# Performance work log

Hardware: AMD Instinct MI355X
Metric: run time of the kernel (lower is better)

The kernel has to match this reference:

```python
import jax, jax.numpy as jnp
import numpy as np

N = 64        # n_nodes per graph
H = 128       # hidden channels (128x0e + 128x1o)
NB = 8        # radial bessel basis size
L = 2         # num_interactions
R_MAX = 5.0
AVG_NEIGH = 63.0
DIM = 3       # output vector dim
B = 64        # batch (vmapped)
T = 32        # time-embedding dim
S = 5         # num_species


def _edges(n):
    # fully-connected graph, no self loops (static shapes, jit-friendly)
    s, r = np.meshgrid(np.arange(n), np.arange(n), indexing='ij')
    m = s != r
    return jnp.asarray(s[m]), jnp.asarray(r[m])


def setup_inputs() -> dict:
    key = jax.random.key(0)
    ks = jax.random.split(key, 12)
    sc = 0.05
    return {
        'positions': jax.random.normal(ks[0], (B, N, 3), jnp.float32),
        'node_features': jax.random.randint(ks[1], (B, N), 0, S).astype(jnp.int64),
        'global_features': jax.random.normal(ks[2], (B, T), jnp.float32),
        'emb': jax.random.normal(ks[3], (S, H), jnp.float32) * sc,
        'Wt': jax.random.normal(ks[4], (T, H), jnp.float32) * sc,
        'Wr1': jax.random.normal(ks[5], (L, NB, H), jnp.float32) * sc,
        'Wr2': jax.random.normal(ks[6], (L, H, H), jnp.float32) * sc,
        'Wupd': jax.random.normal(ks[7], (L, H, H), jnp.float32) * sc,
        'Wmix': jax.random.normal(ks[8], (L, H, H), jnp.float32) * sc,
        'Wg1': jax.random.normal(ks[9], (H, H), jnp.float32) * sc,
        'Wg2': jax.random.normal(ks[10], (H, H), jnp.float32) * sc,
        'final_scaling': jnp.ones((), jnp.float32),
    }


def _call_single(pos, z, t, emb, Wt, Wr1, Wr2, Wupd, Wmix, Wg1, Wg2, final_scaling):
    snd, rcv = _edges(N)
    ev = pos[rcv] - pos[snd]                               # [E,3] edge vectors (gather)
    r = jnp.sqrt(jnp.sum(ev * ev, axis=-1) + 1e-12)        # [E]
    u = ev / r[:, None]                                    # unit directions
    # Bessel radial basis with cosine cutoff (r_max acts as soft radius graph)
    n = jnp.arange(1, NB + 1, dtype=pos.dtype)
    rb = jnp.sin(n * jnp.pi * r[:, None] / R_MAX) / r[:, None]   # [E,NB]
    fc = 0.5 * (jnp.cos(jnp.pi * r / R_MAX) + 1.0) * (r < R_MAX)
    rb = rb * fc[:, None]
    # node embedding from species + time embedding
    h = emb[z] + t @ Wt                                    # [N,H] scalar features
    v = jnp.zeros((N, H, DIM), pos.dtype)                  # vector (1o) features
    for l in range(L):
        w = jax.nn.silu(rb @ Wr1[l]) @ Wr2[l]              # [E,H] radial weights
        m0 = w * h[snd]                                    # [E,H] scalar messages
        m1 = m0[:, :, None] * u[:, None, :]                # [E,H,3] vector messages
        a0 = jax.ops.segment_sum(m0, rcv, num_segments=N) / AVG_NEIGH
        a1 = jax.ops.segment_sum(m1, rcv, num_segments=N) / AVG_NEIGH
        h = h + a0 @ Wupd[l]
        v = v + jnp.einsum('ngd,gh->nhd', a1, Wmix[l])
    # equivariant readout: scalar gate per channel contracts vector channels
    g = jax.nn.silu(h @ Wg1) @ Wg2                         # [N,H]
    out = jnp.einsum('nhd,nh->nd', v, g)                   # [N,3]
    return out * final_scaling


def reference(positions, node_features, global_features, emb, Wt, Wr1, Wr2, Wupd, Wmix, Wg1, Wg2, final_scaling):
    f = lambda p, z, t: _call_single(p, z, t, emb, Wt, Wr1, Wr2, Wupd, Wmix, Wg1, Wg2, final_scaling)
    return jax.vmap(f)(positions, node_features, global_features)
```

## Files before the change

kernel.cpp:

```cpp
#include <hip/hip_runtime.h>
#include <math.h>

#define NN 64
#define HH 128
#define NBB 8
#define TT 32
#define BB 64
#define NROW (BB * NN)
#define PLANE ((size_t)NROW * HH)
#define WR1OFF (8 * 16384)

typedef __attribute__((ext_vector_type(8))) short short8;
typedef __attribute__((ext_vector_type(4))) float f32x4;
typedef __attribute__((ext_vector_type(2))) float f32x2;

__device__ __forceinline__ float silu_f(float x) {
  return x * __builtin_amdgcn_rcpf(1.0f + __expf(-x));
}

__device__ __forceinline__ unsigned short bf1(float x) {
  __bf16 h = (__bf16)x;
  return *(unsigned short*)&h;
}
__device__ __forceinline__ unsigned bf2(float lo, float hi) {
  return (unsigned)bf1(lo) | ((unsigned)bf1(hi) << 16);
}

__device__ __forceinline__ void gemm8(
    const unsigned short (*sA)[136], const unsigned short* __restrict__ Bp,
    int w, int nlo, int quad, f32x4 C[2]) {
  const short8 z8 = {0, 0, 0, 0, 0, 0, 0, 0};
  short8 afr[4];
#pragma unroll
  for (int kt = 0; kt < 4; ++kt)
    afr[kt] = (nlo < 8) ? *(const short8*)&sA[nlo][kt * 32 + quad * 8] : z8;
#pragma unroll
  for (int nt = 0; nt < 2; ++nt)
#pragma unroll
    for (int kt = 0; kt < 4; ++kt) {
      short8 bfr = *(const short8*)&Bp[((kt * 128 + w * 32 + nt * 16 + nlo) * 4 + quad) * 8];
      C[nt] = __builtin_amdgcn_mfma_f32_16x16x32_bf16(afr[kt], bfr, C[nt], 0, 0, 0);
    }
}

__global__ __launch_bounds__(256) void k_init(
    const float* __restrict__ emb, const int* __restrict__ z,
    const float* __restrict__ gf, const float* __restrict__ Wt,
    const float* __restrict__ Wr1, const float* __restrict__ Wr2,
    const float* __restrict__ Wupd, const float* __restrict__ Wmix,
    const float* __restrict__ Wg1, const float* __restrict__ Wg2,
    float* __restrict__ h, unsigned short* __restrict__ Wpack) {
  __shared__ float tvec[HH];
  __shared__ int sz[NN];
  int b4 = blockIdx.x, tid = threadIdx.x;
#pragma unroll
  for (int ii = 0; ii < 2; ++ii) {
    int idx = b4 * 512 + ii * 256 + tid;
    int m = idx >> 14;
    int local = idx & 16383;
    float val;
    if (m < 2) val = Wr2[idx];
    else if (m < 4) val = Wupd[idx - 32768];
    else if (m < 6) val = Wmix[idx - 65536];
    else if (m == 6) val = Wg1[local];
    else val = Wg2[local];
    int k = local >> 7, n = local & 127;
    int kt = k >> 5, q = (k >> 3) & 3, j = k & 7;
    Wpack[(idx & ~16383) + (((kt * 128 + n) * 4 + q) * 8) + j] = bf1(val);
  }
  if (tid < 32) {
    int e = b4 * 32 + tid;
    int l = e >> 12, p = e & 4095;
    int n = p >> 5, q = (p >> 3) & 3, j = p & 7;
    float val = (q == 0) ? Wr1[l * NBB * HH + j * HH + n] : 0.f;
    Wpack[WR1OFF + l * 4096 + p] = bf1(val);
  }
  if (b4 < 64) {
    int b = b4;
    if (tid < NN) sz[tid] = z[b * NN + tid];
    if (tid < HH) {
      float acc = 0.f;
#pragma unroll
      for (int k = 0; k < TT; ++k) acc += gf[b * TT + k] * Wt[k * HH + tid];
      tvec[tid] = acc;
    }
    __syncthreads();
    for (int i = tid; i < NN * HH; i += 256) {
      int n = i >> 7, c = i & 127;
      h[(size_t)b * NN * HH + i] = emb[sz[n] * HH + c] + tvec[c];
    }
  }
}

__global__ __launch_bounds__(256) void k_layer(
    const float* __restrict__ pos,
    const float* __restrict__ hA,
    const unsigned short* __restrict__ a0in,
    unsigned short* __restrict__ apout,
    const unsigned short* __restrict__ Wpack,
    int l) {
  __shared__ __align__(16) unsigned short sh_S[NN][136];
  __shared__ __align__(16) unsigned short sh_rbh[2][NN][8];
  __shared__ __align__(16) float sh_u[2][3][NN];

  int blk = blockIdx.x;
  int b = blk >> 5, rp = blk & 31;
  int r0 = rp * 2;
  int tid = threadIdx.x;
  int w = tid >> 6, lane = tid & 63;
  int nlo = lane & 15, quad = lane >> 4;

  f32x4 hbv[4][2];
#pragma unroll
  for (int mt = 0; mt < 4; ++mt)
#pragma unroll
    for (int nt = 0; nt < 2; ++nt)
#pragma unroll
      for (int reg = 0; reg < 4; ++reg)
        hbv[mt][nt][reg] =
            hA[((size_t)b * NN + mt * 16 + quad * 4 + reg) * HH + w * 32 + nt * 16 + nlo];

  {
    int s = tid & 63;
    int ksel = (tid >> 6) & 1;
    int ri = (tid >> 7) & 1;
    int r = r0 + ri;
    const float* pb = pos + b * NN * 3;
    float dx = pb[r * 3 + 0] - pb[s * 3 + 0];
    float dy = pb[r * 3 + 1] - pb[s * 3 + 1];
    float dz = pb[r * 3 + 2] - pb[s * 3 + 2];
    float rr = sqrtf(dx * dx + dy * dy + dz * dz + 1e-12f);
    float inv = __builtin_amdgcn_rcpf(rr);
    if (ksel == 0) {
      sh_u[ri][0][s] = dx * inv; sh_u[ri][1][s] = dy * inv; sh_u[ri][2][s] = dz * inv;
    }
    const float PI_OVER_5 = 0.628318530717958647692f;
    float fc = (s != r && rr < 5.0f) ? 0.5f * (__cosf(PI_OVER_5 * rr) + 1.0f) : 0.0f;
    float base = PI_OVER_5 * rr;
    float sc = inv * fc;
    int k0 = ksel * 4;
    float v0 = __sinf((float)(k0 + 1) * base) * sc;
    float v1 = __sinf((float)(k0 + 2) * base) * sc;
    float v2 = __sinf((float)(k0 + 3) * base) * sc;
    float v3 = __sinf((float)(k0 + 4) * base) * sc;
    *(unsigned*)&sh_rbh[ri][s][k0]     = bf2(v0, v1);
    *(unsigned*)&sh_rbh[ri][s][k0 + 2] = bf2(v2, v3);
  }
  if (l) {
    for (int i = tid; i < NN * 64; i += 256) {
      int s = i >> 6, c2 = (i & 63) * 2;
      *(unsigned*)&sh_S[s][c2] =
          *(const unsigned*)&a0in[((size_t)b * NN + s) * HH + c2];
    }
  }
  __syncthreads();

  if (l) {
    const unsigned short* Bu = Wpack + 2 * 16384;
#pragma unroll
    for (int mt = 0; mt < 4; ++mt) {
      short8 afr[4];
#pragma unroll
      for (int kt = 0; kt < 4; ++kt)
        afr[kt] = *(const short8*)&sh_S[mt * 16 + nlo][kt * 32 + quad * 8];
#pragma unroll
      for (int nt = 0; nt < 2; ++nt)
#pragma unroll
        for (int kt = 0; kt < 4; ++kt) {
          short8 bfr = *(const short8*)&Bu[((kt * 128 + w * 32 + nt * 16 + nlo) * 4 + quad) * 8];
          hbv[mt][nt] = __builtin_amdgcn_mfma_f32_16x16x32_bf16(afr[kt], bfr, hbv[mt][nt], 0, 0, 0);
        }
    }
    __syncthreads();
  }

  const unsigned short* Wr1p = Wpack + WR1OFF + l * 4096;
  short8 bw[2];
#pragma unroll
  for (int nt = 0; nt < 2; ++nt)
    bw[nt] = *(const short8*)&Wr1p[((w * 32 + nt * 16 + nlo) * 4 + quad) * 8];
  const unsigned short* Bbase = Wpack + l * 16384;
  short8 bfr[4][2];
#pragma unroll
  for (int kt = 0; kt < 4; ++kt)
#pragma unroll
    for (int nt = 0; nt < 2; ++nt)
      bfr[kt][nt] = *(const short8*)&Bbase[((kt * 128 + w * 32 + nt * 16 + nlo) * 4 + quad) * 8];

  const short8 zero8 = {0, 0, 0, 0, 0, 0, 0, 0};
  const float invAvg = 1.0f / 63.0f;

#pragma unroll
  for (int ri = 0; ri < 2; ++ri) {
#pragma unroll
    for (int mtp = 0; mtp < 2; ++mtp) {
      f32x4 Cs[2][2];
#pragma unroll
      for (int mi = 0; mi < 2; ++mi)
#pragma unroll
        for (int nt = 0; nt < 2; ++nt) Cs[mi][nt] = (f32x4){0.f, 0.f, 0.f, 0.f};
#pragma unroll
      for (int mi = 0; mi < 2; ++mi) {
        int mt = mtp * 2 + mi;
        short8 afr = (quad == 0) ? *(const short8*)&sh_rbh[ri][mt * 16 + nlo][0] : zero8;
#pragma unroll
        for (int nt = 0; nt < 2; ++nt)
          Cs[mi][nt] = __builtin_amdgcn_mfma_f32_16x16x32_bf16(afr, bw[nt], Cs[mi][nt], 0, 0, 0);
      }
#pragma unroll
      for (int mi = 0; mi < 2; ++mi)
#pragma unroll
        for (int nt = 0; nt < 2; ++nt)
#pragma unroll
          for (int reg = 0; reg < 4; ++reg) {
            int s = (mtp * 2 + mi) * 16 + quad * 4 + reg;
            int c = w * 32 + nt * 16 + nlo;
            sh_S[s][c] = bf1(silu_f(Cs[mi][nt][reg]));
          }
    }
    __syncthreads();

    float acc0[2] = {0.f, 0.f};
    float a1x[2] = {0.f, 0.f};
    float a1y[2] = {0.f, 0.f};
    float a1z[2] = {0.f, 0.f};
#pragma unroll
    for (int mt = 0; mt < 4; ++mt) {
      short8 afr[4];
      int s_a = mt * 16 + nlo;
#pragma unroll
      for (int kt = 0; kt < 4; ++kt)
        afr[kt] = *(const short8*)&sh_S[s_a][kt * 32 + quad * 8];
      float ux[4], uy[4], uz[4];
#pragma unroll
      for (int reg = 0; reg < 4; ++reg) {
        int s = mt * 16 + quad * 4 + reg;
        ux[reg] = sh_u[ri][0][s]; uy[reg] = sh_u[ri][1][s]; uz[reg] = sh_u[ri][2][s];
      }
#pragma unroll
      for (int nt = 0; nt < 2; ++nt) {
        f32x4 C = {0.f, 0.f, 0.f, 0.f};
#pragma unroll
        for (int kt = 0; kt < 4; ++kt)
          C = __builtin_amdgcn_mfma_f32_16x16x32_bf16(afr[kt], bfr[kt][nt], C, 0, 0, 0);
#pragma unroll
        for (int reg = 0; reg < 4; ++reg) {
          float m0 = C[reg] * hbv[mt][nt][reg];
          acc0[nt] += m0;
          a1x[nt] += m0 * ux[reg];
          a1y[nt] += m0 * uy[reg];
          a1z[nt] += m0 * uz[reg];
        }
      }
    }
#pragma unroll
    for (int nt = 0; nt < 2; ++nt) {
      float q0 = acc0[nt], q1 = a1x[nt], q2 = a1y[nt], q3 = a1z[nt];
      q0 += __shfl_xor(q0, 16); q0 += __shfl_xor(q0, 32);
      q1 += __shfl_xor(q1, 16); q1 += __shfl_xor(q1, 32);
      q2 += __shfl_xor(q2, 16); q2 += __shfl_xor(q2, 32);
      q3 += __shfl_xor(q3, 16); q3 += __shfl_xor(q3, 32);
      if (quad == 0) {
        size_t base = (size_t)(b * NN + r0 + ri) * HH + w * 32 + nt * 16 + nlo;
        apout[(l * 4 + 0) * PLANE + base] = bf1(q0 * invAvg);
        apout[(l * 4 + 1) * PLANE + base] = bf1(q1 * invAvg);
        apout[(l * 4 + 2) * PLANE + base] = bf1(q2 * invAvg);
        apout[(l * 4 + 3) * PLANE + base] = bf1(q3 * invAvg);
      }
    }
    if (ri == 0) __syncthreads();
  }
}

__global__ __launch_bounds__(256) void k_update_ro(
    const unsigned short* __restrict__ apbf, const float* __restrict__ hA,
    const unsigned short* __restrict__ Wpack,
    const float* __restrict__ fs, float* __restrict__ out) {
  __shared__ __align__(16) unsigned short sh_a[8][8][136];
  __shared__ __align__(16) unsigned short sh_h[8][136];
  __shared__ float red[4][8][3];
  int tid = threadIdx.x, w = tid >> 6, lane = tid & 63;
  int nlo = lane & 15, quad = lane >> 4;
  int row0 = blockIdx.x * 8;
  for (int i = tid; i < 8 * 8 * 64; i += 256) {
    int p = i >> 9, rr = (i >> 6) & 7, c2 = (i & 63) * 2;
    *(unsigned*)&sh_a[p][rr][c2] =
        *(const unsigned*)&apbf[p * PLANE + (size_t)(row0 + rr) * HH + c2];
  }
  f32x4 Ch[2];
#pragma unroll
  for (int nt = 0; nt < 2; ++nt)
#pragma unroll
    for (int reg = 0; reg < 4; ++reg)
      Ch[nt][reg] = (quad < 2)
          ? hA[(size_t)(row0 + quad * 4 + reg) * HH + w * 32 + nt * 16 + nlo] : 0.f;
  __syncthreads();
  gemm8(sh_a[0], Wpack + 2 * 16384, w, nlo, quad, Ch);
  gemm8(sh_a[4], Wpack + 3 * 16384, w, nlo, quad, Ch);
  f32x4 Cx[2] = {{0,0,0,0},{0,0,0,0}};
  f32x4 Cy[2] = {{0,0,0,0},{0,0,0,0}};
  f32x4 Cz[2] = {{0,0,0,0},{0,0,0,0}};
  gemm8(sh_a[1], Wpack + 4 * 16384, w, nlo, quad, Cx);
  gemm8(sh_a[5], Wpack + 5 * 16384, w, nlo, quad, Cx);
  gemm8(sh_a[2], Wpack + 4 * 16384, w, nlo, quad, Cy);
  gemm8(sh_a[6], Wpack + 5 * 16384, w, nlo, quad, Cy);
  gemm8(sh_a[3], Wpack + 4 * 16384, w, nlo, quad, Cz);
  gemm8(sh_a[7], Wpack + 5 * 16384, w, nlo, quad, Cz);
  if (quad < 2) {
#pragma unroll
    for (int nt = 0; nt < 2; ++nt)
#pragma unroll
      for (int reg = 0; reg < 4; ++reg)
        sh_h[quad * 4 + reg][w * 32 + nt * 16 + nlo] = bf1(Ch[nt][reg]);
  }
  __syncthreads();
  unsigned short (*sh_q)[136] = sh_a[0];
  f32x4 Cq[2] = {{0,0,0,0},{0,0,0,0}};
  gemm8(sh_h, Wpack + 6 * 16384, w, nlo, quad, Cq);
  if (quad < 2) {
#pragma unroll
    for (int nt = 0; nt < 2; ++nt)
#pragma unroll
      for (int reg = 0; reg < 4; ++reg)
        sh_q[quad * 4 + reg][w * 32 + nt * 16 + nlo] = bf1(silu_f(Cq[nt][reg]));
  }
  __syncthreads();
  f32x4 Cg[2] = {{0,0,0,0},{0,0,0,0}};
  gemm8(sh_q, Wpack + 7 * 16384, w, nlo, quad, Cg);
  float pr[3][4];
#pragma unroll
  for (int d = 0; d < 3; ++d)
#pragma unroll
    for (int reg = 0; reg < 4; ++reg) pr[d][reg] = 0.f;
#pragma unroll
  for (int nt = 0; nt < 2; ++nt)
#pragma unroll
    for (int reg = 0; reg < 4; ++reg) {
      float gv = Cg[nt][reg];
      pr[0][reg] += gv * Cx[nt][reg];
      pr[1][reg] += gv * Cy[nt][reg];
      pr[2][reg] += gv * Cz[nt][reg];
    }
#pragma unroll
  for (int off = 1; off < 16; off <<= 1)
#pragma unroll
    for (int d = 0; d < 3; ++d)
#pragma unroll
      for (int reg = 0; reg < 4; ++reg)
        pr[d][reg] += __shfl_xor(pr[d][reg], off);
  if (nlo == 0 && quad < 2) {
#pragma unroll
    for (int d = 0; d < 3; ++d)
#pragma unroll
      for (int reg = 0; reg < 4; ++reg)
        red[w][quad * 4 + reg][d] = pr[d][reg];
  }
  __syncthreads();
  if (tid < 24) {
    int row = tid / 3, d = tid % 3;
    float s = red[0][row][d] + red[1][row][d] + red[2][row][d] + red[3][row][d];
    out[(size_t)(row0 + row) * 3 + d] = s * fs[0];
  }
}

extern "C" void kernel_launch(void* const* d_in, const int* in_sizes, int n_in,
                              void* d_out, int out_size, void* d_ws, size_t ws_size,
                              hipStream_t stream) {
  const float* pos  = (const float*)d_in[0];
  const int*   z    = (const int*)d_in[1];
  const float* gf   = (const float*)d_in[2];
  const float* emb  = (const float*)d_in[3];
  const float* Wt   = (const float*)d_in[4];
  const float* Wr1  = (const float*)d_in[5];
  const float* Wr2  = (const float*)d_in[6];
  const float* Wupd = (const float*)d_in[7];
  const float* Wmix = (const float*)d_in[8];
  const float* Wg1  = (const float*)d_in[9];
  const float* Wg2  = (const float*)d_in[10];
  const float* fs   = (const float*)d_in[11];
  float* out = (float*)d_out;

  float* ws = (float*)d_ws;
  float* hA = ws;
  unsigned short* apbf = (unsigned short*)(ws + PLANE);
  unsigned short* Wpack = (unsigned short*)(ws + 5 * PLANE);

  k_init<<<dim3(256), dim3(256), 0, stream>>>(emb, z, gf, Wt, Wr1, Wr2, Wupd,
                                              Wmix, Wg1, Wg2, hA, Wpack);
  k_layer<<<dim3(BB * 32), dim3(256), 0, stream>>>(pos, hA, apbf, apbf, Wpack, 0);
  k_layer<<<dim3(BB * 32), dim3(256), 0, stream>>>(pos, hA, apbf, apbf, Wpack, 1);
  k_update_ro<<<dim3(512), dim3(256), 0, stream>>>(apbf, hA, Wpack, fs, out);
}
```

Measured before the change: 158.0 us.

## Compute segment-sum aggregations with an MFMA over bf16 messages instead of scalar reductions

Per-edge scalar messages are now converted to bf16 and written transposed into a per-wave shared tile. A second MFMA then contracts them against a small matrix of [1/avg, ux/avg, uy/avg, uz/avg] unit vectors. This replaces the per-lane FMA accumulation and the cross-lane shuffle reduction for the four aggregated outputs. In exchange it adds extra shared-memory traffic and rounds the messages and directions to bf16 before summing, which reduces accuracy.

```diff
diff --git a/kernel.cpp b/kernel.cpp
--- a/kernel.cpp
+++ b/kernel.cpp
@@ -13,6 +13,7 @@
 typedef __attribute__((ext_vector_type(8))) short short8;
 typedef __attribute__((ext_vector_type(4))) float f32x4;
 typedef __attribute__((ext_vector_type(2))) float f32x2;
+typedef __attribute__((ext_vector_type(2))) unsigned int u32x2;
 
 __device__ __forceinline__ float silu_f(float x) {
   return x * __builtin_amdgcn_rcpf(1.0f + __expf(-x));
@@ -100,8 +101,9 @@
     const unsigned short* __restrict__ Wpack,
     int l) {
   __shared__ __align__(16) unsigned short sh_S[NN][136];
+  __shared__ __align__(16) unsigned short sh_M0T[4][32][72];
   __shared__ __align__(16) unsigned short sh_rbh[2][NN][8];
-  __shared__ __align__(16) float sh_u[2][3][NN];
+  __shared__ __align__(16) unsigned short sh_ub[2][4][NN];
 
   int blk = blockIdx.x;
   int b = blk >> 5, rp = blk & 31;
@@ -131,8 +133,14 @@
     float dz = pb[r * 3 + 2] - pb[s * 3 + 2];
     float rr = sqrtf(dx * dx + dy * dy + dz * dz + 1e-12f);
     float inv = __builtin_amdgcn_rcpf(rr);
+    const float invAvg = 1.0f / 63.0f;
     if (ksel == 0) {
-      sh_u[ri][0][s] = dx * inv; sh_u[ri][1][s] = dy * inv; sh_u[ri][2][s] = dz * inv;
+      float ia = inv * invAvg;
+      sh_ub[ri][1][s] = bf1(dx * ia);
+      sh_ub[ri][2][s] = bf1(dy * ia);
+      sh_ub[ri][3][s] = bf1(dz * ia);
+    } else {
+      sh_ub[ri][0][s] = bf1(invAvg);
     }
     const float PI_OVER_5 = 0.628318530717958647692f;
     float fc = (s != r && rr < 5.0f) ? 0.5f * (__cosf(PI_OVER_5 * rr) + 1.0f) : 0.0f;
@@ -188,7 +196,12 @@
       bfr[kt][nt] = *(const short8*)&Bbase[((kt * 128 + w * 32 + nt * 16 + nlo) * 4 + quad) * 8];
 
   const short8 zero8 = {0, 0, 0, 0, 0, 0, 0, 0};
-  const float invAvg = 1.0f / 63.0f;
+  short8 au[2][2];
+#pragma unroll
+  for (int ri = 0; ri < 2; ++ri)
+#pragma unroll
+    for (int kt = 0; kt < 2; ++kt)
+      au[ri][kt] = (nlo < 4) ? *(const short8*)&sh_ub[ri][nlo][kt * 32 + quad * 8] : zero8;
 
 #pragma unroll
   for (int ri = 0; ri < 2; ++ri) {
@@ -220,10 +233,6 @@
     }
     __syncthreads();
 
-    float acc0[2] = {0.f, 0.f};
-    float a1x[2] = {0.f, 0.f};
-    float a1y[2] = {0.f, 0.f};
-    float a1z[2] = {0.f, 0.f};
 #pragma unroll
     for (int mt = 0; mt < 4; ++mt) {
       short8 afr[4];
@@ -231,41 +240,36 @@
 #pragma unroll
       for (int kt = 0; kt < 4; ++kt)
         afr[kt] = *(const short8*)&sh_S[s_a][kt * 32 + quad * 8];
-      float ux[4], uy[4], uz[4];
-#pragma unroll
-      for (int reg = 0; reg < 4; ++reg) {
-        int s = mt * 16 + quad * 4 + reg;
-        ux[reg] = sh_u[ri][0][s]; uy[reg] = sh_u[ri][1][s]; uz[reg] = sh_u[ri][2][s];
-      }
 #pragma unroll
       for (int nt = 0; nt < 2; ++nt) {
         f32x4 C = {0.f, 0.f, 0.f, 0.f};
 #pragma unroll
         for (int kt = 0; kt < 4; ++kt)
           C = __builtin_amdgcn_mfma_f32_16x16x32_bf16(afr[kt], bfr[kt][nt], C, 0, 0, 0);
-#pragma unroll
-        for (int reg = 0; reg < 4; ++reg) {
-          float m0 = C[reg] * hbv[mt][nt][reg];
-          acc0[nt] += m0;
-          a1x[nt] += m0 * ux[reg];
-          a1y[nt] += m0 * uy[reg];
-          a1z[nt] += m0 * uz[reg];
+        f32x4 m0 = C * hbv[mt][nt];
+        u32x2 pk;
+        pk.x = bf2(m0[0], m0[1]);
+        pk.y = bf2(m0[2], m0[3]);
+        *(u32x2*)&sh_M0T[w][nt * 16 + nlo][mt * 16 + quad * 4] = pk;
+      }
+    }
+    {
+      f32x4 Cu[2] = {{0, 0, 0, 0}, {0, 0, 0, 0}};
+#pragma unroll
+      for (int nt = 0; nt < 2; ++nt)
+#pragma unroll
+        for (int kt = 0; kt < 2; ++kt) {
+          short8 bm = *(const short8*)&sh_M0T[w][nt * 16 + nlo][kt * 32 + quad * 8];
+          Cu[nt] = __builtin_amdgcn_mfma_f32_16x16x32_bf16(au[ri][kt], bm, Cu[nt], 0, 0, 0);
         }
-      }
-    }
-#pragma unroll
-    for (int nt = 0; nt < 2; ++nt) {
-      float q0 = acc0[nt], q1 = a1x[nt], q2 = a1y[nt], q3 = a1z[nt];
-      q0 += __shfl_xor(q0, 16); q0 += __shfl_xor(q0, 32);
-      q1 += __shfl_xor(q1, 16); q1 += __shfl_xor(q1, 32);
-      q2 += __shfl_xor(q2, 16); q2 += __shfl_xor(q2, 32);
-      q3 += __shfl_xor(q3, 16); q3 += __shfl_xor(q3, 32);
       if (quad == 0) {
-        size_t base = (size_t)(b * NN + r0 + ri) * HH + w * 32 + nt * 16 + nlo;
-        apout[(l * 4 + 0) * PLANE + base] = bf1(q0 * invAvg);
-        apout[(l * 4 + 1) * PLANE + base] = bf1(q1 * invAvg);
-        apout[(l * 4 + 2) * PLANE + base] = bf1(q2 * invAvg);
-        apout[(l * 4 + 3) * PLANE + base] = bf1(q3 * invAvg);
+#pragma unroll
+        for (int nt = 0; nt < 2; ++nt) {
+          size_t base = (size_t)(b * NN + r0 + ri) * HH + w * 32 + nt * 16 + nlo;
+#pragma unroll
+          for (int reg = 0; reg < 4; ++reg)
+            apout[(l * 4 + reg) * PLANE + base] = bf1(Cu[nt][reg]);
+        }
       }
     }
     if (ri == 0) __syncthreads();
```

Result: faster. 152.8 us (-3.3%).
